# Optimization experiments

Measured on AMD Instinct MI355X. Metric: run time of the kernel, lower is better.

The kernel has to match this reference:

```python
import jax, jax.numpy as jnp
import numpy as np

B, T, ICD, H = 64, 256, 2000, 384
L, CH, W = 3, H // 3, 10  # levels, chunk_size, conv window


def setup_inputs() -> dict:
    key = jax.random.key(0)
    ks = jax.random.split(key, 10)
    s = 0.05
    return {
        "x": jax.random.uniform(ks[0], (B, T, ICD), jnp.float32),
        "dia_w": jax.random.normal(ks[1], (ICD, H), jnp.float32) * s,
        "dia_b": jnp.zeros((H,), jnp.float32),
        "kernel_w": jax.random.normal(ks[2], (H + 1, 4 * H + 2 * L), jnp.float32) * s,
        "kernel_b": jnp.zeros((4 * H + 2 * L,), jnp.float32),
        "rec_w": jax.random.normal(ks[3], (H + 1, 4 * H + 2 * L), jnp.float32) * s,
        "rec_b": jnp.zeros((4 * H + 2 * L,), jnp.float32),
        "scale_w": jax.random.normal(ks[4], (H, H // 6), jnp.float32) * s,
        "scale_b": jnp.zeros((H // 6,), jnp.float32),
        "rescale_w": jax.random.normal(ks[5], (H // 6, H), jnp.float32) * s,
        "rescale_b": jnp.zeros((H,), jnp.float32),
        "conv_w": jax.random.normal(ks[6], (H, H, W), jnp.float32) * s,  # (out, in, k)
        "conv_b": jnp.zeros((H,), jnp.float32),
        "out_w": jax.random.normal(ks[7], (H, ICD), jnp.float32) * s,
        "out_b": jnp.zeros((ICD,), jnp.float32),
        "choice": 0,  # 0 == 'dia'
    }


def _cumax_l2r(x):
    return jnp.cumsum(jax.nn.softmax(x, -1), -1)


def _cumax_r2l(x):
    return jnp.flip(jnp.cumsum(jax.nn.softmax(jnp.flip(x, -1), -1), -1), -1)


def _forward(x, dia_w, dia_b, kernel_w, kernel_b, rec_w, rec_b,
             scale_w, scale_b, rescale_w, rescale_b, conv_w, conv_b,
             out_w, out_b):
    embed = x @ dia_w + dia_b  # (B,T,H), choice='dia'
    Bs = embed.shape[0]
    ones = jnp.ones((Bs, 1), embed.dtype)  # interval T == 1

    def step(carry, xt):
        c, h, tmp_h, tmp_dis = carry
        xo = (jnp.concatenate([xt, ones], -1) @ kernel_w + kernel_b
              + jnp.concatenate([h, ones], -1) @ rec_w + rec_b)
        fm = _cumax_l2r(xo[:, :L])[:, :, None]          # (B,L,1)
        im = _cumax_r2l(xo[:, L:2 * L])[:, :, None]     # (B,L,1)
        g = xo[:, 2 * L:].reshape(Bs, 4 * L, CH)
        f = jax.nn.sigmoid(g[:, :L])
        i = jax.nn.sigmoid(g[:, L:2 * L])
        o = jax.nn.sigmoid(g[:, 2 * L:3 * L])
        c_in = jnp.tanh(g[:, 3 * L:])
        c_last = c.reshape(Bs, L, CH)
        ov = fm * im
        c_new = ov * (f * c_last + i * c_in) + (fm - ov) * c_last + (im - ov) * c_in
        h_new = (o * jnp.tanh(c_new)).reshape(Bs, H)
        c_new = c_new.reshape(Bs, H)
        cur_dis = 1.0 - jnp.mean(fm[..., 0], -1)        # (B,)
        tmp_h = jnp.concatenate([tmp_h[1:], h_new[None]], 0)      # (W,B,H)
        tmp_dis = jnp.concatenate([tmp_dis[1:], cur_dis[None]], 0)  # (W,B)
        local_dis = jax.nn.softmax(jnp.cumsum(tmp_dis.T, 1), 1)   # (B,W)
        local_h = tmp_h.transpose(1, 2, 0) * local_dis[:, None, :]  # (B,H,W)
        theme = jax.nn.sigmoid(
            jax.nn.relu(jnp.mean(local_h, -1) @ scale_w + scale_b) @ rescale_w + rescale_b)
        conv = jnp.einsum('bhw,ohw->bo', local_h, conv_w) + conv_b  # Conv1d, full-width kernel
        return (c_new, h_new, tmp_h, tmp_dis), (h_new, theme * conv)

    carry0 = (jnp.zeros((Bs, H), embed.dtype), jnp.zeros((Bs, H), embed.dtype),
              jnp.zeros((W, Bs, H), embed.dtype), jnp.zeros((W, Bs), embed.dtype))
    _, (origin_h, loc_h) = jax.lax.scan(step, carry0, embed.transpose(1, 0, 2))
    rnn = (origin_h + loc_h).transpose(1, 0, 2)  # (B,T,H); dropout off (eval)
    return rnn @ out_w + out_b                   # (B,T,ICD)


def reference(x, dia_w, dia_b, kernel_w, kernel_b, rec_w, rec_b,
              scale_w, scale_b, rescale_w, rescale_b, conv_w, conv_b,
              out_w, out_b, choice):
    # choice==0 -> 'dia' embedding path
    return _forward(x, dia_w, dia_b, kernel_w, kernel_b, rec_w, rec_b,
                    scale_w, scale_b, rescale_w, rescale_b, conv_w, conv_b,
                    out_w, out_b)
```

## Files before the change

### kernel.cpp

```cpp
#include <hip/hip_runtime.h>
#include <hip/hip_bf16.h>
#include <cstdint>
#include <cstddef>

#define B_DIM   64
#define T_DIM   256
#define ICD_DIM 2000
#define H_DIM   384
#define CH_DIM  128
#define W_WIN   10
#define M_DIM   (B_DIM * T_DIM)
#define XO_DIM  1542
#define XO_PAD  1664
#define K_X     2016
#define KCONV   3840
#define N_OUTP  2048

typedef unsigned short ushort_t;
typedef unsigned int   uint_t;
typedef __attribute__((ext_vector_type(8))) short short8;
typedef __attribute__((ext_vector_type(4))) float f32x4;
typedef __attribute__((ext_vector_type(2))) _Float16 f16x2;

__device__ __forceinline__ ushort_t f2bf(float v) {
    __hip_bfloat16 b = __float2bfloat16(v);
    ushort_t u; __builtin_memcpy(&u, &b, 2); return u;
}
__device__ __forceinline__ float bf2f(ushort_t u) {
    __hip_bfloat16 b; __builtin_memcpy(&b, &u, 2); return __bfloat162float(b);
}
__device__ __forceinline__ uint_t pk2bf(float a, float b) {
    return (uint_t)f2bf(a) | ((uint_t)f2bf(b) << 16);
}
__device__ __forceinline__ float sigmoidf_(float x) { return 1.f / (1.f + expf(-x)); }
__device__ __forceinline__ f16x2 asf16x2(uint_t u) { f16x2 h; __builtin_memcpy(&h, &u, 4); return h; }
__device__ __forceinline__ uint_t pkf16(float a, float b) {
    f16x2 h; h.x = (_Float16)a; h.y = (_Float16)b;
    uint_t u; __builtin_memcpy(&u, &h, 4); return u;
}
__device__ __forceinline__ float dot2f(uint_t a, uint_t b, float acc) {
#if __has_builtin(__builtin_amdgcn_fdot2)
    return __builtin_amdgcn_fdot2(asf16x2(a), asf16x2(b), acc, false);
#else
    f16x2 ha = asf16x2(a), hb = asf16x2(b);
    return acc + (float)ha.x * (float)hb.x + (float)ha.y * (float)hb.y;
#endif
}

#define GLOAD_LDS16(g, l) __builtin_amdgcn_global_load_lds( \
    (const __attribute__((address_space(1))) void*)(g),     \
    (__attribute__((address_space(3))) void*)(l), 16, 0, 0)

__global__ void prep_x(const float* __restrict__ x, ushort_t* __restrict__ xb)
{
    int id = blockIdx.x * 256 + threadIdx.x;
    if (id >= M_DIM * (K_X / 8)) return;
    const int m = id / (K_X / 8), c = id - m * (K_X / 8);
    const int k = c * 8;
    uint_t o[4];
    if (k + 7 < ICD_DIM) {
        const float* p = x + (size_t)m * ICD_DIM + k;
        const float4 a = *(const float4*)p;
        const float4 b = *(const float4*)(p + 4);
        o[0] = pk2bf(a.x, a.y); o[1] = pk2bf(a.z, a.w);
        o[2] = pk2bf(b.x, b.y); o[3] = pk2bf(b.z, b.w);
    } else {
        float v[8];
#pragma unroll
        for (int i = 0; i < 8; ++i)
            v[i] = (k + i < ICD_DIM) ? x[(size_t)m * ICD_DIM + k + i] : 0.f;
        o[0] = pk2bf(v[0], v[1]); o[1] = pk2bf(v[2], v[3]);
        o[2] = pk2bf(v[4], v[5]); o[3] = pk2bf(v[6], v[7]);
    }
    *(uint4*)&xb[(size_t)m * K_X + k] = make_uint4(o[0], o[1], o[2], o[3]);
}
__global__ void prep_dia(const float* __restrict__ dia_w, ushort_t* __restrict__ hi)
{
    int id = blockIdx.x * 256 + threadIdx.x;
    if (id >= H_DIM * K_X) return;
    int n = id / K_X, k = id - n * K_X;
    hi[id] = f2bf((k < ICD_DIM) ? dia_w[(size_t)k * H_DIM + n] : 0.f);
}
__global__ void prep_ker(const float* __restrict__ kernel_w, ushort_t* __restrict__ hi)
{
    int id = blockIdx.x * 256 + threadIdx.x;
    if (id >= XO_PAD * H_DIM) return;
    int n = id / H_DIM, k = id - n * H_DIM;
    hi[id] = f2bf((n < XO_DIM) ? kernel_w[(size_t)k * XO_DIM + n] : 0.f);
}
__global__ void prep_conv(const float* __restrict__ conv_w, ushort_t* __restrict__ bt)
{
    int id = blockIdx.x * 256 + threadIdx.x;
    if (id >= H_DIM * KCONV) return;
    int o = id / KCONV, k = id - o * KCONV;
    int w = k / H_DIM, h = k - w * H_DIM;
    bt[id] = f2bf(conv_w[((size_t)o * H_DIM + h) * W_WIN + w]);
}
__global__ void prep_out(const float* __restrict__ out_w, ushort_t* __restrict__ bt)
{
    int id = blockIdx.x * 256 + threadIdx.x;
    if (id >= N_OUTP * H_DIM) return;
    int n = id / H_DIM, k = id - n * H_DIM;
    bt[id] = f2bf((n < ICD_DIM) ? out_w[(size_t)k * ICD_DIM + n] : 0.f);
}
__global__ void prep_misc(const float* __restrict__ kernel_w, const float* __restrict__ kernel_b,
                          const float* __restrict__ rec_w, const float* __restrict__ rec_b,
                          const float* __restrict__ out_b,
                          float* __restrict__ bias2p, float* __restrict__ outbp)
{
    int j = blockIdx.x * 256 + threadIdx.x;
    if (j < XO_PAD)
        bias2p[j] = (j < XO_DIM) ? (kernel_w[(size_t)H_DIM * XO_DIM + j] + kernel_b[j]
                                  + rec_w[(size_t)H_DIM * XO_DIM + j] + rec_b[j]) : 0.f;
    if (j < N_OUTP)
        outbp[j] = (j < ICD_DIM) ? out_b[j] : 0.f;
}
__global__ void prep_rec2(const float* __restrict__ rec_w, uint_t* __restrict__ recg, uint_t* __restrict__ recm)
{
    int id = blockIdx.x * 256 + threadIdx.x;
    const int NG = 4 * 2 * 96 * 384;
    if (id < NG) {
        int cg = id % 384;
        int kk = (id / 384) % 96;
        int half = (id / (384 * 96)) & 1;
        int q = id / (384 * 96 * 2);
        int p = half * 96 + kk;
        int j = 6 + (cg >> 5) * 128 + q * 32 + (cg & 31);
        recg[id] = pkf16(rec_w[(size_t)(2 * p) * XO_DIM + j], rec_w[(size_t)(2 * p + 1) * XO_DIM + j]);
    } else if (id < NG + 6 * 192) {
        int id2 = id - NG;
        int mc = id2 / 192, p = id2 % 192;
        recm[id2] = pkf16(rec_w[(size_t)(2 * p) * XO_DIM + mc], rec_w[(size_t)(2 * p + 1) * XO_DIM + mc]);
    }
}

template<int MODE>
__global__ __launch_bounds__(256)
void mfma_gemm(const ushort_t* __restrict__ Ab,
               const ushort_t* __restrict__ Bh,
               ushort_t* __restrict__ Cb,
               ushort_t* __restrict__ Ehi, ushort_t* __restrict__ Elo,
               const float* __restrict__ bias,
               const ushort_t* __restrict__ theme,
               const float* __restrict__ hall, const float* __restrict__ ldwp,
               int ksteps, int kdim, int astride)
{
    __shared__ ushort_t AhS[4096];
    __shared__ ushort_t BhS[4096];

    const int tid = threadIdx.x;
    const int rc = tid & 127, kh = tid >> 7;
    const int m0 = blockIdx.y * 128, n0 = blockIdx.x * 128;
    const int kq0 = kh * 2;

    const int lane = tid & 63, wid = tid >> 6;
    const int wm = wid >> 1, wn = wid & 1;
    const int l15 = lane & 15, lkq = lane >> 4;

    f32x4 acc[4][4];
#pragma unroll
    for (int i = 0; i < 4; ++i)
#pragma unroll
        for (int j = 0; j < 4; ++j)
#pragma unroll
            for (int q = 0; q < 4; ++q) acc[i][j][q] = 0.f;

    for (int ks = 0; ks < ksteps; ++ks) {
        const int k16 = ks * 32 + kh * 16;
        __syncthreads();

        if constexpr (MODE == 0) {
            const ushort_t* ap = Ab + (size_t)(m0 + rc) * astride + k16;
            GLOAD_LDS16(ap,     &AhS[(kq0 * 128 + rc) * 8]);
            GLOAD_LDS16(ap + 8, &AhS[((kq0 + 1) * 128 + rc) * 8]);
        } else {
            float v[16];
            const int w = k16 / H_DIM, h0i = k16 - (k16 / H_DIM) * H_DIM;
            const int gm = m0 + rc, b = gm >> 8, tt = gm & 255;
            const int tp = tt - (W_WIN - 1) + w;
            const bool ok = (tp >= 0);
            if (ok) {
                const float lw = ldwp[(size_t)gm * W_WIN + w];
                const float* ap = hall + ((size_t)(b * T_DIM + tp)) * H_DIM + h0i;
#pragma unroll
                for (int q = 0; q < 4; ++q) {
                    float4 t = *(const float4*)(ap + q * 4);
                    v[q * 4 + 0] = t.x * lw; v[q * 4 + 1] = t.y * lw;
                    v[q * 4 + 2] = t.z * lw; v[q * 4 + 3] = t.w * lw;
                }
            } else {
#pragma unroll
                for (int q = 0; q < 16; ++q) v[q] = 0.f;
            }
            uint_t hh[8];
#pragma unroll
            for (int i = 0; i < 8; ++i)
                hh[i] = pk2bf(v[2 * i], v[2 * i + 1]);
            *(uint4*)&AhS[(kq0 * 128 + rc) * 8]       = make_uint4(hh[0], hh[1], hh[2], hh[3]);
            *(uint4*)&AhS[((kq0 + 1) * 128 + rc) * 8] = make_uint4(hh[4], hh[5], hh[6], hh[7]);
        }

        {
            const ushort_t* bp = Bh + (size_t)(n0 + rc) * kdim + k16;
            GLOAD_LDS16(bp,     &BhS[(kq0 * 128 + rc) * 8]);
            GLOAD_LDS16(bp + 8, &BhS[((kq0 + 1) * 128 + rc) * 8]);
        }
        __syncthreads();

        short8 ah[4], bh[4];
#pragma unroll
        for (int mf = 0; mf < 4; ++mf)
            ah[mf] = *(const short8*)&AhS[(lkq * 128 + wm * 64 + mf * 16 + l15) * 8];
#pragma unroll
        for (int nf = 0; nf < 4; ++nf)
            bh[nf] = *(const short8*)&BhS[(lkq * 128 + wn * 64 + nf * 16 + l15) * 8];
#pragma unroll
        for (int mf = 0; mf < 4; ++mf)
#pragma unroll
            for (int nf = 0; nf < 4; ++nf)
                acc[mf][nf] = __builtin_amdgcn_mfma_f32_16x16x32_bf16(ah[mf], bh[nf], acc[mf][nf], 0, 0, 0);
    }

#pragma unroll
    for (int mf = 0; mf < 4; ++mf)
#pragma unroll
        for (int nf = 0; nf < 4; ++nf)
#pragma unroll
            for (int j = 0; j < 4; ++j) {
                const int gm = m0 + wm * 64 + mf * 16 + lkq * 4 + j;
                const int gn = n0 + wn * 64 + nf * 16 + l15;
                float v = acc[mf][nf][j] + bias[gn];
                if constexpr (MODE == 0) {
                    ushort_t h = f2bf(v);
                    Ehi[(size_t)gm * H_DIM + gn] = h;
                    Elo[(size_t)gm * H_DIM + gn] = f2bf(v - bf2f(h));
                } else {
                    const size_t ix = (size_t)gm * H_DIM + gn;
                    v = v * bf2f(theme[ix]) + hall[ix];
                    Cb[ix] = f2bf(v);
                }
            }
}

template<int MODE>
__global__ __launch_bounds__(512)
void mfma_gemm256(const ushort_t* __restrict__ Ah, const ushort_t* __restrict__ Al,
                  const ushort_t* __restrict__ Bm, float* __restrict__ Cf,
                  const float* __restrict__ bias,
                  int ksteps, int kdim, int astride, int ncols, int cld)
{
    constexpr bool SPLITA = (MODE == 1);
    __shared__ ushort_t AhS[8192];
    __shared__ ushort_t AlS[SPLITA ? 8192 : 16];
    __shared__ ushort_t BhS[4096];

    const int tid = threadIdx.x;
    const int m0 = blockIdx.y * 256, n0 = blockIdx.x * 128;

    const int arow = tid & 255, akh = tid >> 8;
    const int akq0 = akh * 2;
    const int bcol = tid & 127, bkq = tid >> 7;

    const int lane = tid & 63, wid = tid >> 6;
    const int wm = wid >> 1, wn = wid & 1;
    const int l15 = lane & 15, lkq = lane >> 4;

    f32x4 acc[4][4];
#pragma unroll
    for (int i = 0; i < 4; ++i)
#pragma unroll
        for (int j = 0; j < 4; ++j)
#pragma unroll
            for (int q = 0; q < 4; ++q) acc[i][j][q] = 0.f;

    for (int ks = 0; ks < ksteps; ++ks) {
        const int kb = ks * 32;
        __syncthreads();
        {
            const ushort_t* ap = Ah + (size_t)(m0 + arow) * astride + kb + akh * 16;
            GLOAD_LDS16(ap,     &AhS[((akq0 + 0) * 256 + arow) * 8]);
            GLOAD_LDS16(ap + 8, &AhS[((akq0 + 1) * 256 + arow) * 8]);
            if constexpr (SPLITA) {
                const ushort_t* ap2 = Al + (size_t)(m0 + arow) * astride + kb + akh * 16;
                GLOAD_LDS16(ap2,     &AlS[((akq0 + 0) * 256 + arow) * 8]);
                GLOAD_LDS16(ap2 + 8, &AlS[((akq0 + 1) * 256 + arow) * 8]);
            }
        }
        {
            const ushort_t* bp = Bm + (size_t)(n0 + bcol) * kdim + kb + bkq * 8;
            GLOAD_LDS16(bp, &BhS[(bkq * 128 + bcol) * 8]);
        }
        __syncthreads();

        short8 ah[4], al[4], bh[4];
#pragma unroll
        for (int mf = 0; mf < 4; ++mf)
            ah[mf] = *(const short8*)&AhS[(lkq * 256 + wm * 64 + mf * 16 + l15) * 8];
#pragma unroll
        for (int nf = 0; nf < 4; ++nf)
            bh[nf] = *(const short8*)&BhS[(lkq * 128 + wn * 64 + nf * 16 + l15) * 8];
        if constexpr (SPLITA) {
#pragma unroll
            for (int mf = 0; mf < 4; ++mf)
                al[mf] = *(const short8*)&AlS[(lkq * 256 + wm * 64 + mf * 16 + l15) * 8];
        }
#pragma unroll
        for (int mf = 0; mf < 4; ++mf)
#pragma unroll
            for (int nf = 0; nf < 4; ++nf) {
                acc[mf][nf] = __builtin_amdgcn_mfma_f32_16x16x32_bf16(ah[mf], bh[nf], acc[mf][nf], 0, 0, 0);
                if constexpr (SPLITA)
                    acc[mf][nf] = __builtin_amdgcn_mfma_f32_16x16x32_bf16(al[mf], bh[nf], acc[mf][nf], 0, 0, 0);
            }
    }

#pragma unroll
    for (int mf = 0; mf < 4; ++mf)
#pragma unroll
        for (int nf = 0; nf < 4; ++nf)
#pragma unroll
            for (int j = 0; j < 4; ++j) {
                const int gm = m0 + wm * 64 + mf * 16 + lkq * 4 + j;
                const int gn = n0 + wn * 64 + nf * 16 + l15;
                if (gn < ncols)
                    Cf[(size_t)gm * cld + gn] = acc[mf][nf][j] + bias[gn];
            }
}

__global__ __launch_bounds__(768, 3)
void scan_kernel(const float* __restrict__ Xproj, const uint_t* __restrict__ recg,
                 const uint_t* __restrict__ recm, float* __restrict__ h_all,
                 float* __restrict__ dis_all, uint_t* __restrict__ hpk)
{
    __shared__ ushort_t hs16[H_DIM];
    __shared__ float xo_s[384];
    __shared__ uint_t wm2[6 * 192];
    __shared__ float c_s[96];
    __shared__ float fm_s[3], im_s[3];

    const int tid = threadIdx.x;
    const int q = blockIdx.x >> 6, b = blockIdx.x & 63;

    const int cg = tid >> 1, half = tid & 1;
    const int jg = 6 + (cg >> 5) * 128 + q * 32 + (cg & 31);

    const int gl = tid / 32, gu = tid & 31;
    const int jglob = gl * 128 + q * 32 + gu;

    const int rsp = tid - 96;
    const int qq_sp = (q + 1 + rsp / 96) & 3;
    const int s_sp = rsp % 96;
    const int j_sp = (s_sp >> 5) * 128 + qq_sp * 32 + (s_sp & 31);

    for (int i = tid; i < 6 * 192; i += 768) wm2[i] = recm[i];
    if (tid < H_DIM) hs16[tid] = 0;
    if (tid < 96) c_s[tid] = 0.f;

    uint_t w[96];
#pragma unroll
    for (int kk = 0; kk < 96; ++kk)
        w[kk] = recg[(size_t)((q * 2 + half) * 96 + kk) * 384 + cg];

    float xv = 0.f, xvm = 0.f;
    if (half == 0) xv = Xproj[((size_t)b * T_DIM + 0) * XO_DIM + jg];
    if (tid < 24 && (tid & 3) == 0) xvm = Xproj[((size_t)b * T_DIM + 0) * XO_DIM + (tid >> 2)];

    __syncthreads();

    for (int t = 0; t < T_DIM; ++t) {
        {
            float acc = 0.f;
            const ushort_t* hp = &hs16[half * 192];
#pragma unroll
            for (int kk = 0; kk < 96; kk += 4) {
                const uint4 hq = *(const uint4*)(hp + kk * 2);
                acc = dot2f(w[kk + 0], hq.x, acc);
                acc = dot2f(w[kk + 1], hq.y, acc);
                acc = dot2f(w[kk + 2], hq.z, acc);
                acc = dot2f(w[kk + 3], hq.w, acc);
            }
            acc += __shfl_xor(acc, 1);
            if (half == 0) xo_s[cg] = acc + xv;
        }

        if (tid < 64) {
            float acc = 0.f;
            if (tid < 24) {
                const int mc = tid >> 2, kq = tid & 3;
                const uint_t* wp = &wm2[mc * 192 + kq * 48];
#pragma unroll
                for (int kk = 0; kk < 48; kk += 4) {
                    const uint4 hq = *(const uint4*)&hs16[(kq * 48 + kk) * 2];
                    acc = dot2f(wp[kk + 0], hq.x, acc);
                    acc = dot2f(wp[kk + 1], hq.y, acc);
                    acc = dot2f(wp[kk + 2], hq.z, acc);
                    acc = dot2f(wp[kk + 3], hq.w, acc);
                }
                if ((tid & 3) == 0) acc += xvm;
            }
            acc += __shfl_xor(acc, 2);
            acc += __shfl_xor(acc, 1);
            const float m0 = __shfl(acc, 0),  m1 = __shfl(acc, 4),  m2 = __shfl(acc, 8);
            const float m3 = __shfl(acc, 12), m4 = __shfl(acc, 16), m5 = __shfl(acc, 20);
            if (tid == 0) {
                float mx = fmaxf(m0, fmaxf(m1, m2));
                float e0 = expf(m0 - mx), e1 = expf(m1 - mx), e2 = expf(m2 - mx);
                float inv = 1.f / (e0 + e1 + e2);
                const float f0 = e0 * inv, f1 = (e0 + e1) * inv;
                fm_s[0] = f0; fm_s[1] = f1; fm_s[2] = 1.f;
                mx = fmaxf(m3, fmaxf(m4, m5));
                e0 = expf(m3 - mx); e1 = expf(m4 - mx); e2 = expf(m5 - mx);
                inv = 1.f / (e0 + e1 + e2);
                im_s[0] = 1.f; im_s[1] = (e1 + e2) * inv; im_s[2] = e2 * inv;
                if (q == 0)
                    dis_all[b * T_DIM + t] = 1.f - (f0 + f1 + 1.f) * (1.f / 3.f);
            }
        }
        __syncthreads();

        if (tid < 96) {
            const float fm = fm_s[gl], im = im_s[gl];
            const float fg = sigmoidf_(xo_s[gl * 32 + gu]);
            const float ig = sigmoidf_(xo_s[(3 + gl) * 32 + gu]);
            const float og = sigmoidf_(xo_s[(6 + gl) * 32 + gu]);
            const float ci = tanhf(xo_s[(9 + gl) * 32 + gu]);
            const float cl = c_s[tid];
            const float ov = fm * im;
            const float cn = ov * (fg * cl + ig * ci) + (fm - ov) * cl + (im - ov) * ci;
            const float hn = og * tanhf(cn);
            _Float16 hf = (_Float16)hn;
            ushort_t hb; __builtin_memcpy(&hb, &hf, 2);
            const uint_t word = ((uint_t)hb << 16) | (uint_t)(t + 1);
            __hip_atomic_store(&hpk[(size_t)(t & 1) * B_DIM * H_DIM + b * H_DIM + jglob],
                               word, __ATOMIC_RELAXED, __HIP_MEMORY_SCOPE_AGENT);
            c_s[tid] = cn;
            hs16[jglob] = hb;
            h_all[((size_t)b * T_DIM + t) * H_DIM + jglob] = hn;
        }

        if (t + 1 < T_DIM) {
            if (half == 0) xv = Xproj[((size_t)b * T_DIM + (t + 1)) * XO_DIM + jg];
            if (tid < 24 && (tid & 3) == 0) xvm = Xproj[((size_t)b * T_DIM + (t + 1)) * XO_DIM + (tid >> 2)];
        }

        if (t + 1 < T_DIM) {
            if (tid >= 96 && tid < 384) {
                const uint_t want = (uint_t)(t + 1);
                uint_t* addr = &hpk[(size_t)(t & 1) * B_DIM * H_DIM + b * H_DIM + j_sp];
                uint_t v = __hip_atomic_load(addr, __ATOMIC_RELAXED, __HIP_MEMORY_SCOPE_AGENT);
                while ((v & 0xFFFFu) != want) {
                    __builtin_amdgcn_s_sleep(1);
                    v = __hip_atomic_load(addr, __ATOMIC_RELAXED, __HIP_MEMORY_SCOPE_AGENT);
                }
                hs16[j_sp] = (ushort_t)(v >> 16);
            }
            __syncthreads();
        }
    }
}

__global__ __launch_bounds__(256, 2)
void locdis2_kernel(const float* __restrict__ h_all, const float* __restrict__ dis_all,
                    const float* __restrict__ scale_w, const float* __restrict__ scale_b,
                    const float* __restrict__ rescale_w, const float* __restrict__ rescale_b,
                    float* __restrict__ ldw, ushort_t* __restrict__ theme)
{
    __shared__ float ring[10][H_DIM];
    __shared__ float ld_all[64][10];
    __shared__ uint_t mh2[192];
    __shared__ float part_s[4][64];
    __shared__ float hid[64];
    __shared__ uint_t hid2[32];

    const int tid = threadIdx.x;
    const int b = blockIdx.x >> 2, t0 = (blockIdx.x & 3) * 64;

    const int o1 = tid & 63, p1 = tid >> 6;
    uint_t w1[48];
#pragma unroll
    for (int kk = 0; kk < 48; ++kk) {
        const int p = p1 * 48 + kk;
        w1[kk] = pkf16(scale_w[(size_t)(2 * p) * 64 + o1], scale_w[(size_t)(2 * p + 1) * 64 + o1]);
    }
    uint_t w2[48];
#pragma unroll
    for (int j = 0; j < 3; ++j) {
        const int o2 = j * 128 + (tid >> 1), hf = tid & 1;
#pragma unroll
        for (int kk = 0; kk < 16; ++kk) {
            const int p = hf * 16 + kk;
            w2[j * 16 + kk] = pkf16(rescale_w[(size_t)(2 * p) * H_DIM + o2],
                                    rescale_w[(size_t)(2 * p + 1) * H_DIM + o2]);
        }
    }

    if (tid < 64) {
        const int t = t0 + tid;
        float cum = 0.f, c[10];
        for (int wq = 0; wq < 10; ++wq) {
            const int tp = t - 9 + wq;
            cum += (tp >= 0) ? dis_all[b * T_DIM + tp] : 0.f;
            c[wq] = cum;
        }
        float mx = c[0];
        for (int wq = 1; wq < 10; ++wq) mx = fmaxf(mx, c[wq]);
        float s = 0.f, e[10];
        for (int wq = 0; wq < 10; ++wq) { e[wq] = expf(c[wq] - mx); s += e[wq]; }
        const float inv = 1.f / s;
        for (int wq = 0; wq < 10; ++wq) {
            ld_all[tid][wq] = e[wq] * inv;
            ldw[((size_t)b * T_DIM + t) * W_WIN + wq] = e[wq] * inv;
        }
    }
    for (int tp = t0 - 9; tp < t0; ++tp) {
        if (tp >= 0) {
            for (int i = tid; i < H_DIM; i += 256)
                ring[tp % 10][i] = h_all[((size_t)b * T_DIM + tp) * H_DIM + i];
        }
    }
    __syncthreads();

    for (int r = 0; r < 64; ++r) {
        const int t = t0 + r;
        if (tid < 192) {
            const float2 h2 = *(const float2*)&h_all[((size_t)b * T_DIM + t) * H_DIM + 2 * tid];
            *(float2*)&ring[t % 10][2 * tid] = h2;
        }
        __syncthreads();
        if (tid < 192) {
            float a0 = 0.f, a1 = 0.f;
            for (int wq = 0; wq < 10; ++wq) {
                const int tp = t - 9 + wq;
                if (tp >= 0) {
                    const float lw = ld_all[r][wq];
                    a0 += lw * ring[tp % 10][2 * tid];
                    a1 += lw * ring[tp % 10][2 * tid + 1];
                }
            }
            mh2[tid] = pkf16(a0 * 0.1f, a1 * 0.1f);
        }
        __syncthreads();
        {
            float acc = 0.f;
#pragma unroll
            for (int kk = 0; kk < 48; ++kk)
                acc = dot2f(w1[kk], mh2[p1 * 48 + kk], acc);
            part_s[p1][o1] = acc;
        }
        __syncthreads();
        if (tid < 64)
            hid[tid] = fmaxf(scale_b[tid] + part_s[0][tid] + part_s[1][tid] + part_s[2][tid] + part_s[3][tid], 0.f);
        __syncthreads();
        if (tid < 32) hid2[tid] = pkf16(hid[2 * tid], hid[2 * tid + 1]);
        __syncthreads();
#pragma unroll
        for (int j = 0; j < 3; ++j) {
            const int o2 = j * 128 + (tid >> 1), hf = tid & 1;
            float acc = 0.f;
#pragma unroll
            for (int kk = 0; kk < 16; ++kk)
                acc = dot2f(w2[j * 16 + kk], hid2[hf * 16 + kk], acc);
            acc += __shfl_xor(acc, 1);
            if (hf == 0)
                theme[((size_t)b * T_DIM + t) * H_DIM + o2] = f2bf(sigmoidf_(acc + rescale_b[o2]));
        }
        __syncthreads();
    }
}

extern "C" void kernel_launch(void* const* d_in, const int* in_sizes, int n_in,
                              void* d_out, int out_size, void* d_ws, size_t ws_size,
                              hipStream_t stream)
{
    const float* x         = (const float*)d_in[0];
    const float* dia_w     = (const float*)d_in[1];
    const float* dia_b     = (const float*)d_in[2];
    const float* kernel_w  = (const float*)d_in[3];
    const float* kernel_b  = (const float*)d_in[4];
    const float* rec_w     = (const float*)d_in[5];
    const float* rec_b     = (const float*)d_in[6];
    const float* scale_w   = (const float*)d_in[7];
    const float* scale_b   = (const float*)d_in[8];
    const float* rescale_w = (const float*)d_in[9];
    const float* rescale_b = (const float*)d_in[10];
    const float* conv_w    = (const float*)d_in[11];
    const float* conv_b    = (const float*)d_in[12];
    const float* out_w     = (const float*)d_in[13];
    const float* out_b     = (const float*)d_in[14];
    (void)in_sizes; (void)n_in; (void)out_size; (void)ws_size;

    float* ws = (float*)d_ws;
    size_t off = 0;
    float* Xproj   = ws + off; off += (size_t)M_DIM * XO_DIM;
    float* h_all   = ws + off; off += (size_t)M_DIM * H_DIM;
    float* ldw     = ws + off; off += (size_t)M_DIM * W_WIN;
    float* dis_all = ws + off; off += M_DIM;
    float* bias2p  = ws + off; off += XO_PAD;
    float* outbp   = ws + off; off += N_OUTP;
    uint_t* hpk    = (uint_t*)(ws + off); off += (size_t)2 * B_DIM * H_DIM;
    ushort_t* us = (ushort_t*)(ws + off);
    size_t uo = 0;
    ushort_t* dia_hi = us + uo; uo += (size_t)H_DIM * K_X;
    ushort_t* ker_hi = us + uo; uo += (size_t)XO_PAD * H_DIM;
    ushort_t* conv_t = us + uo; uo += (size_t)H_DIM * KCONV;
    ushort_t* outw_t = us + uo; uo += (size_t)N_OUTP * H_DIM;
    ushort_t* ehi    = us + uo; uo += (size_t)M_DIM * H_DIM;
    ushort_t* elo    = us + uo; uo += (size_t)M_DIM * H_DIM;
    ushort_t* themeb = us + uo; uo += (size_t)M_DIM * H_DIM;
    ushort_t* rnnb   = us + uo; uo += (size_t)M_DIM * H_DIM;
    uint_t* recg = (uint_t*)(us + uo); uo += (size_t)2 * 4 * 2 * 96 * 384;
    uint_t* recm = (uint_t*)(us + uo); uo += (size_t)2 * 6 * 192;

    ushort_t* xb = (ushort_t*)Xproj;

    prep_x   <<<(M_DIM * (K_X / 8) + 255) / 256, 256, 0, stream>>>(x, xb);
    prep_dia <<<(H_DIM * K_X + 255) / 256, 256, 0, stream>>>(dia_w, dia_hi);
    prep_ker <<<(XO_PAD * H_DIM + 255) / 256, 256, 0, stream>>>(kernel_w, ker_hi);
    prep_conv<<<(H_DIM * KCONV + 255) / 256, 256, 0, stream>>>(conv_w, conv_t);
    prep_out <<<(N_OUTP * H_DIM + 255) / 256, 256, 0, stream>>>(out_w, outw_t);
    prep_misc<<<(N_OUTP + 255) / 256, 256, 0, stream>>>(kernel_w, kernel_b, rec_w, rec_b, out_b, bias2p, outbp);
    prep_rec2<<<(4 * 2 * 96 * 384 + 6 * 192 + 255) / 256, 256, 0, stream>>>(rec_w, recg, recm);

    mfma_gemm<0><<<dim3(3, 128), 256, 0, stream>>>(
        xb, dia_hi, nullptr, ehi, elo,
        dia_b, nullptr, nullptr, nullptr, K_X / 32, K_X, K_X);

    mfma_gemm256<1><<<dim3(13, 64), 512, 0, stream>>>(
        ehi, elo, ker_hi, Xproj, bias2p, H_DIM / 32, H_DIM, H_DIM, XO_DIM, XO_DIM);

    {
        void* args[] = { (void*)&Xproj, (void*)&recg, (void*)&recm,
                         (void*)&h_all, (void*)&dis_all, (void*)&hpk };
        (void)hipLaunchCooperativeKernel((const void*)scan_kernel, dim3(256), dim3(768), args, 0, stream);
    }

    locdis2_kernel<<<256, 256, 0, stream>>>(
        h_all, dis_all, scale_w, scale_b, rescale_w, rescale_b, ldw, themeb);

    mfma_gemm<2><<<dim3(3, 128), 256, 0, stream>>>(
        nullptr, conv_t, rnnb, nullptr, nullptr,
        conv_b, themeb, h_all, ldw, KCONV / 32, KCONV, 0);

    mfma_gemm256<3><<<dim3(16, 64), 512, 0, stream>>>(
        rnnb, nullptr, outw_t, (float*)d_out, outbp, H_DIM / 32, H_DIM, H_DIM, ICD_DIM, ICD_DIM);
}
```

Baseline: 1.356 ms.

## Merge weight prep kernels, hoist conv-window weights, and spin before sleeping

Six separate weight-preparation launches become one kernel that picks its task by index range, cutting launch overhead and the gaps between launches. In the MODE 2 GEMM, each thread loads its ten local-distance weights and row base pointer once before the k-loop instead of recomputing them every k-step, and converts straight to packed bf16. The scan's spin-wait now polls once before its first sleep, which should shorten the handoff delay between timesteps. The merged kernel adds branch divergence at the range boundaries, and the hoisted array raises register pressure.

```diff
diff --git a/kernel.cpp b/kernel.cpp
--- a/kernel.cpp
+++ b/kernel.cpp
@@ -74,52 +74,62 @@
     }
     *(uint4*)&xb[(size_t)m * K_X + k] = make_uint4(o[0], o[1], o[2], o[3]);
 }
-__global__ void prep_dia(const float* __restrict__ dia_w, ushort_t* __restrict__ hi)
+
+#define PW_S0 (H_DIM * K_X)
+#define PW_S1 (XO_PAD * H_DIM)
+#define PW_S2 (H_DIM * KCONV)
+#define PW_S3 (N_OUTP * H_DIM)
+#define PW_S4 (N_OUTP)
+#define PW_S5 (4 * 2 * 96 * 384)
+#define PW_S6 (6 * 192)
+#define PW_TOT (PW_S0 + PW_S1 + PW_S2 + PW_S3 + PW_S4 + PW_S5 + PW_S6)
+
+__global__ void prep_weights(const float* __restrict__ dia_w, const float* __restrict__ kernel_w,
+                             const float* __restrict__ rec_w, const float* __restrict__ conv_w,
+                             const float* __restrict__ out_w,
+                             const float* __restrict__ kernel_b, const float* __restrict__ rec_b,
+                             const float* __restrict__ out_b,
+                             ushort_t* __restrict__ dia_hi, ushort_t* __restrict__ ker_hi,
+                             ushort_t* __restrict__ conv_t, ushort_t* __restrict__ outw_t,
+                             float* __restrict__ bias2p, float* __restrict__ outbp,
+                             uint_t* __restrict__ recg, uint_t* __restrict__ recm)
 {
     int id = blockIdx.x * 256 + threadIdx.x;
-    if (id >= H_DIM * K_X) return;
-    int n = id / K_X, k = id - n * K_X;
-    hi[id] = f2bf((k < ICD_DIM) ? dia_w[(size_t)k * H_DIM + n] : 0.f);
-}
-__global__ void prep_ker(const float* __restrict__ kernel_w, ushort_t* __restrict__ hi)
-{
-    int id = blockIdx.x * 256 + threadIdx.x;
-    if (id >= XO_PAD * H_DIM) return;
-    int n = id / H_DIM, k = id - n * H_DIM;
-    hi[id] = f2bf((n < XO_DIM) ? kernel_w[(size_t)k * XO_DIM + n] : 0.f);
-}
-__global__ void prep_conv(const float* __restrict__ conv_w, ushort_t* __restrict__ bt)
-{
-    int id = blockIdx.x * 256 + threadIdx.x;
-    if (id >= H_DIM * KCONV) return;
-    int o = id / KCONV, k = id - o * KCONV;
-    int w = k / H_DIM, h = k - w * H_DIM;
-    bt[id] = f2bf(conv_w[((size_t)o * H_DIM + h) * W_WIN + w]);
-}
-__global__ void prep_out(const float* __restrict__ out_w, ushort_t* __restrict__ bt)
-{
-    int id = blockIdx.x * 256 + threadIdx.x;
-    if (id >= N_OUTP * H_DIM) return;
-    int n = id / H_DIM, k = id - n * H_DIM;
-    bt[id] = f2bf((n < ICD_DIM) ? out_w[(size_t)k * ICD_DIM + n] : 0.f);
-}
-__global__ void prep_misc(const float* __restrict__ kernel_w, const float* __restrict__ kernel_b,
-                          const float* __restrict__ rec_w, const float* __restrict__ rec_b,
-                          const float* __restrict__ out_b,
-                          float* __restrict__ bias2p, float* __restrict__ outbp)
-{
-    int j = blockIdx.x * 256 + threadIdx.x;
-    if (j < XO_PAD)
-        bias2p[j] = (j < XO_DIM) ? (kernel_w[(size_t)H_DIM * XO_DIM + j] + kernel_b[j]
-                                  + rec_w[(size_t)H_DIM * XO_DIM + j] + rec_b[j]) : 0.f;
-    if (j < N_OUTP)
+    if (id < PW_S0) {
+        int n = id / K_X, k = id - n * K_X;
+        dia_hi[id] = f2bf((k < ICD_DIM) ? dia_w[(size_t)k * H_DIM + n] : 0.f);
+        return;
+    }
+    id -= PW_S0;
+    if (id < PW_S1) {
+        int n = id / H_DIM, k = id - n * H_DIM;
+        ker_hi[id] = f2bf((n < XO_DIM) ? kernel_w[(size_t)k * XO_DIM + n] : 0.f);
+        return;
+    }
+    id -= PW_S1;
+    if (id < PW_S2) {
+        int o = id / KCONV, k = id - o * KCONV;
+        int w = k / H_DIM, h = k - w * H_DIM;
+        conv_t[id] = f2bf(conv_w[((size_t)o * H_DIM + h) * W_WIN + w]);
+        return;
+    }
+    id -= PW_S2;
+    if (id < PW_S3) {
+        int n = id / H_DIM, k = id - n * H_DIM;
+        outw_t[id] = f2bf((n < ICD_DIM) ? out_w[(size_t)k * ICD_DIM + n] : 0.f);
+        return;
+    }
+    id -= PW_S3;
+    if (id < PW_S4) {
+        int j = id;
+        if (j < XO_PAD)
+            bias2p[j] = (j < XO_DIM) ? (kernel_w[(size_t)H_DIM * XO_DIM + j] + kernel_b[j]
+                                      + rec_w[(size_t)H_DIM * XO_DIM + j] + rec_b[j]) : 0.f;
         outbp[j] = (j < ICD_DIM) ? out_b[j] : 0.f;
-}
-__global__ void prep_rec2(const float* __restrict__ rec_w, uint_t* __restrict__ recg, uint_t* __restrict__ recm)
-{
-    int id = blockIdx.x * 256 + threadIdx.x;
-    const int NG = 4 * 2 * 96 * 384;
-    if (id < NG) {
+        return;
+    }
+    id -= PW_S4;
+    if (id < PW_S5) {
         int cg = id % 384;
         int kk = (id / 384) % 96;
         int half = (id / (384 * 96)) & 1;
@@ -127,10 +137,12 @@
         int p = half * 96 + kk;
         int j = 6 + (cg >> 5) * 128 + q * 32 + (cg & 31);
         recg[id] = pkf16(rec_w[(size_t)(2 * p) * XO_DIM + j], rec_w[(size_t)(2 * p + 1) * XO_DIM + j]);
-    } else if (id < NG + 6 * 192) {
-        int id2 = id - NG;
-        int mc = id2 / 192, p = id2 % 192;
-        recm[id2] = pkf16(rec_w[(size_t)(2 * p) * XO_DIM + mc], rec_w[(size_t)(2 * p + 1) * XO_DIM + mc]);
+        return;
+    }
+    id -= PW_S5;
+    if (id < PW_S6) {
+        int mc = id / 192, p = id % 192;
+        recm[id] = pkf16(rec_w[(size_t)(2 * p) * XO_DIM + mc], rec_w[(size_t)(2 * p + 1) * XO_DIM + mc]);
     }
 }
 
@@ -157,6 +169,17 @@
     const int wm = wid >> 1, wn = wid & 1;
     const int l15 = lane & 15, lkq = lane >> 4;
 
+    float lw10[10];
+    const float* hrow = nullptr;
+    int tt_m2 = 0;
+    if constexpr (MODE == 2) {
+        const int gm = m0 + rc, b = gm >> 8;
+        tt_m2 = gm & 255;
+        hrow = hall + ((size_t)(b * T_DIM + tt_m2) - (W_WIN - 1)) * H_DIM;
+#pragma unroll
+        for (int w = 0; w < 10; ++w) lw10[w] = ldwp[(size_t)gm * W_WIN + w];
+    }
+
     f32x4 acc[4][4];
 #pragma unroll
     for (int i = 0; i < 4; ++i)
@@ -174,28 +197,21 @@
             GLOAD_LDS16(ap,     &AhS[(kq0 * 128 + rc) * 8]);
             GLOAD_LDS16(ap + 8, &AhS[((kq0 + 1) * 128 + rc) * 8]);
         } else {
-            float v[16];
-            const int w = k16 / H_DIM, h0i = k16 - (k16 / H_DIM) * H_DIM;
-            const int gm = m0 + rc, b = gm >> 8, tt = gm & 255;
-            const int tp = tt - (W_WIN - 1) + w;
-            const bool ok = (tp >= 0);
-            if (ok) {
-                const float lw = ldwp[(size_t)gm * W_WIN + w];
-                const float* ap = hall + ((size_t)(b * T_DIM + tp)) * H_DIM + h0i;
-#pragma unroll
-                for (int q = 0; q < 4; ++q) {
-                    float4 t = *(const float4*)(ap + q * 4);
-                    v[q * 4 + 0] = t.x * lw; v[q * 4 + 1] = t.y * lw;
-                    v[q * 4 + 2] = t.z * lw; v[q * 4 + 3] = t.w * lw;
+            const int w = k16 / H_DIM;
+            uint_t hh[8];
+            if (tt_m2 + w >= W_WIN - 1) {
+                const float lw = lw10[w];
+                const float* ap = hrow + k16;
+#pragma unroll
+                for (int qq = 0; qq < 4; ++qq) {
+                    float4 t = *(const float4*)(ap + qq * 4);
+                    hh[qq * 2]     = pk2bf(t.x * lw, t.y * lw);
+                    hh[qq * 2 + 1] = pk2bf(t.z * lw, t.w * lw);
                 }
             } else {
 #pragma unroll
-                for (int q = 0; q < 16; ++q) v[q] = 0.f;
-            }
-            uint_t hh[8];
-#pragma unroll
-            for (int i = 0; i < 8; ++i)
-                hh[i] = pk2bf(v[2 * i], v[2 * i + 1]);
+                for (int i = 0; i < 8; ++i) hh[i] = 0u;
+            }
             *(uint4*)&AhS[(kq0 * 128 + rc) * 8]       = make_uint4(hh[0], hh[1], hh[2], hh[3]);
             *(uint4*)&AhS[((kq0 + 1) * 128 + rc) * 8] = make_uint4(hh[4], hh[5], hh[6], hh[7]);
         }
@@ -448,8 +464,9 @@
                 const uint_t want = (uint_t)(t + 1);
                 uint_t* addr = &hpk[(size_t)(t & 1) * B_DIM * H_DIM + b * H_DIM + j_sp];
                 uint_t v = __hip_atomic_load(addr, __ATOMIC_RELAXED, __HIP_MEMORY_SCOPE_AGENT);
+                int k = 0;
                 while ((v & 0xFFFFu) != want) {
-                    __builtin_amdgcn_s_sleep(1);
+                    if (k++ > 0) __builtin_amdgcn_s_sleep(1);
                     v = __hip_atomic_load(addr, __ATOMIC_RELAXED, __HIP_MEMORY_SCOPE_AGENT);
                 }
                 hs16[j_sp] = (ushort_t)(v >> 16);
@@ -613,13 +630,10 @@
 
     ushort_t* xb = (ushort_t*)Xproj;
 
-    prep_x   <<<(M_DIM * (K_X / 8) + 255) / 256, 256, 0, stream>>>(x, xb);
-    prep_dia <<<(H_DIM * K_X + 255) / 256, 256, 0, stream>>>(dia_w, dia_hi);
-    prep_ker <<<(XO_PAD * H_DIM + 255) / 256, 256, 0, stream>>>(kernel_w, ker_hi);
-    prep_conv<<<(H_DIM * KCONV + 255) / 256, 256, 0, stream>>>(conv_w, conv_t);
-    prep_out <<<(N_OUTP * H_DIM + 255) / 256, 256, 0, stream>>>(out_w, outw_t);
-    prep_misc<<<(N_OUTP + 255) / 256, 256, 0, stream>>>(kernel_w, kernel_b, rec_w, rec_b, out_b, bias2p, outbp);
-    prep_rec2<<<(4 * 2 * 96 * 384 + 6 * 192 + 255) / 256, 256, 0, stream>>>(rec_w, recg, recm);
+    prep_x      <<<(M_DIM * (K_X / 8) + 255) / 256, 256, 0, stream>>>(x, xb);
+    prep_weights<<<(PW_TOT + 255) / 256, 256, 0, stream>>>(
+        dia_w, kernel_w, rec_w, conv_w, out_w, kernel_b, rec_b, out_b,
+        dia_hi, ker_hi, conv_t, outw_t, bias2p, outbp, recg, recm);
 
     mfma_gemm<0><<<dim3(3, 128), 256, 0, stream>>>(
         xb, dia_hi, nullptr, ehi, elo,
```

Result: faster. 1.319 ms (-2.7%).
